# Kernel tuning notes

Measured on AMD Instinct MI355X. Metric: run time of the kernel, lower is better.

## Reference

```python
import jax, jax.numpy as jnp
import numpy as np

NUM_HEADS = 16


def setup_inputs() -> dict:
    key = jax.random.key(0)
    ks = jax.random.split(key, 9)
    B, S, C = 2, 2048, 1024
    s = 1.0 / np.sqrt(C)
    return {
        "hidden_states": jax.random.normal(ks[0], (B, S, C), jnp.float32),
        "Wq": jax.random.normal(ks[1], (C, C), jnp.float32) * s,
        "bq": jnp.zeros((C,), jnp.float32),
        "Wk": jax.random.normal(ks[2], (C, C), jnp.float32) * s,
        "bk": jnp.zeros((C,), jnp.float32),
        "Wv": jax.random.normal(ks[3], (C, C), jnp.float32) * s,
        "bv": jnp.zeros((C,), jnp.float32),
        "Wo": jax.random.normal(ks[4], (C, C), jnp.float32) * s,
        "bo": jnp.zeros((C,), jnp.float32),
    }


def reference(hidden_states, Wq, bq, Wk, bk, Wv, bv, Wo, bo):
    # Self-attention path of AttnProcessor (3D input, no mask, no norms,
    # residual_connection=True, rescale_output_factor=1.0).
    B, S, C = hidden_states.shape
    H = NUM_HEADS
    D = C // H
    residual = hidden_states

    q = hidden_states @ Wq + bq  # [B,S,C]
    k = hidden_states @ Wk + bk
    v = hidden_states @ Wv + bv

    # head_to_batch_dim: [B,S,C] -> [B,S,H,D]
    q = q.reshape(B, S, H, D)
    k = k.reshape(B, S, H, D)
    v = v.reshape(B, S, H, D)

    scale = 1.0 / np.sqrt(D).astype(np.float32)
    # get_attention_scores: baddbmm with scale, then softmax (full [B,H,S,S])
    scores = jnp.einsum("bqhd,bkhd->bhqk", q, k) * scale
    probs = jax.nn.softmax(scores, axis=-1)

    out = jnp.einsum("bhqk,bkhd->bqhd", probs, v)  # bmm(probs, value)
    out = out.reshape(B, S, C)  # batch_to_head_dim

    out = out @ Wo + bo  # to_out[0]; to_out[1] is dropout (identity in eval)
    out = out + residual  # residual_connection
    return out  # rescale_output_factor = 1.0
```

## Files before the change

### kernel.cpp

```cpp
#include <hip/hip_runtime.h>

#define BATCH 2
#define SEQ   2048
#define CH    1024
#define NHEAD 16
#define HDIM  64
#define MROWS (BATCH * SEQ)

typedef __attribute__((ext_vector_type(8))) short short8;
typedef __attribute__((ext_vector_type(4))) float floatx4;
typedef unsigned short ushort_t;

__device__ __forceinline__ float b2f(ushort_t u) {
    union { unsigned int i; float f; } x;
    x.i = ((unsigned int)u) << 16;
    return x.f;
}
__device__ __forceinline__ ushort_t f2b(float f) {
    union { float f; unsigned int i; } x;
    x.f = f;
    unsigned int lsb = (x.i >> 16) & 1u;
    x.i += 0x7fffu + lsb;
    return (ushort_t)(x.i >> 16);
}
__device__ __forceinline__ unsigned pack2(float a, float b) {
    return (unsigned)f2b(a) | ((unsigned)f2b(b) << 16);
}

__device__ __forceinline__ void gld16(const ushort_t* g, ushort_t* l) {
    __builtin_amdgcn_global_load_lds(
        (const __attribute__((address_space(1))) void*)g,
        (__attribute__((address_space(3))) void*)l, 16, 0, 0);
}

__global__ __launch_bounds__(256) void cvt_bf16_kernel(
    const float* __restrict__ in, ushort_t* __restrict__ out, int n4) {
    int i = blockIdx.x * blockDim.x + threadIdx.x;
    if (i < n4) {
        float4 v = ((const float4*)in)[i];
        ushort4 o = {f2b(v.x), f2b(v.y), f2b(v.z), f2b(v.w)};
        ((ushort4*)out)[i] = o;
    }
}

__global__ __launch_bounds__(256) void transpose_cvt_all(
    const float* __restrict__ W0, const float* __restrict__ W1,
    const float* __restrict__ W2, const float* __restrict__ W3,
    ushort_t* __restrict__ T0, ushort_t* __restrict__ T1,
    ushort_t* __restrict__ T2, ushort_t* __restrict__ T3) {
    __shared__ ushort_t T[64][68];
    const int z = blockIdx.z;
    const float* W = (z == 0) ? W0 : (z == 1) ? W1 : (z == 2) ? W2 : W3;
    ushort_t* Wt = (z == 0) ? T0 : (z == 1) ? T1 : (z == 2) ? T2 : T3;
    const int tid = threadIdx.x;
    const int n0 = blockIdx.x * 64, k0 = blockIdx.y * 64;
    const int r = tid >> 4, c4 = (tid & 15) * 4;
#pragma unroll
    for (int p = 0; p < 4; p++) {
        int k = p * 16 + r;
        float4 v = *(const float4*)&W[(size_t)(k0 + k) * CH + n0 + c4];
        T[c4 + 0][k] = f2b(v.x);
        T[c4 + 1][k] = f2b(v.y);
        T[c4 + 2][k] = f2b(v.z);
        T[c4 + 3][k] = f2b(v.w);
    }
    __syncthreads();
#pragma unroll
    for (int p = 0; p < 4; p++) {
        int n = p * 16 + r;
        ushort4 o = {T[n][c4 + 0], T[n][c4 + 1], T[n][c4 + 2], T[n][c4 + 3]};
        *(ushort4*)&Wt[(size_t)(n0 + n) * CH + k0 + c4] = o;
    }
}

__device__ __forceinline__ void gemm_core_db(
    const ushort_t* __restrict__ A, const ushort_t* __restrict__ Bt,
    int bm, int n0, int tid, floatx4 acc[4][4], ushort_t* lds) {
    const int wave = tid >> 6, lane = tid & 63;
    const int quad = lane >> 4, t16 = lane & 15;
    const int wm = wave >> 1, wn = wave & 1;
    const int arow = tid >> 2, ak = (tid & 3) * 8;

    const ushort_t* a0 = A + (size_t)(bm + arow) * CH + ak;
    const ushort_t* a1 = A + (size_t)(bm + 64 + arow) * CH + ak;
    const ushort_t* b0 = Bt + (size_t)(n0 + arow) * CH + ak;
    const ushort_t* b1 = Bt + (size_t)(n0 + 64 + arow) * CH + ak;

#pragma unroll
    for (int i = 0; i < 4; i++)
#pragma unroll
        for (int j = 0; j < 4; j++) acc[i][j] = (floatx4){0.f, 0.f, 0.f, 0.f};

    {
        ushort_t* As = lds;
        ushort_t* Bs = lds + 4096;
        gld16(a0, As + wave * 512);
        gld16(a1, As + 2048 + wave * 512);
        gld16(b0, Bs + wave * 512);
        gld16(b1, Bs + 2048 + wave * 512);
    }

    for (int it = 0; it < CH / 32; ++it) {
        __syncthreads();
        if (it + 1 < CH / 32) {
            ushort_t* nAs = lds + ((it + 1) & 1) * 8192;
            ushort_t* nBs = nAs + 4096;
            const int k = (it + 1) * 32;
            gld16(a0 + k, nAs + wave * 512);
            gld16(a1 + k, nAs + 2048 + wave * 512);
            gld16(b0 + k, nBs + wave * 512);
            gld16(b1 + k, nBs + 2048 + wave * 512);
        }
        const ushort_t* As = lds + (it & 1) * 8192;
        const ushort_t* Bs = As + 4096;
        short8 af[4], bf[4];
#pragma unroll
        for (int i = 0; i < 4; i++)
            af[i] = *(const short8*)&As[(wm * 64 + i * 16 + t16) * 32 + quad * 8];
#pragma unroll
        for (int j = 0; j < 4; j++)
            bf[j] = *(const short8*)&Bs[(wn * 64 + j * 16 + t16) * 32 + quad * 8];
#pragma unroll
        for (int i = 0; i < 4; i++)
#pragma unroll
            for (int j = 0; j < 4; j++)
                acc[i][j] = __builtin_amdgcn_mfma_f32_16x16x32_bf16(
                    af[i], bf[j], acc[i][j], 0, 0, 0);
    }
}

__global__ __launch_bounds__(256) void gemm_qkv(
    const ushort_t* __restrict__ X,
    const ushort_t* __restrict__ WqT, const ushort_t* __restrict__ WkT,
    const ushort_t* __restrict__ WvT,
    const float* __restrict__ bq, const float* __restrict__ bk,
    const float* __restrict__ bv,
    ushort_t* __restrict__ Qm, ushort_t* __restrict__ Km,
    ushort_t* __restrict__ Vtm) {
    __shared__ ushort_t lds[2 * 8192];
    const int tid = threadIdx.x;
    const int seg = blockIdx.x >> 3;
    const int n0 = (blockIdx.x & 7) * 128;
    const int bm = blockIdx.y * 128;
    const ushort_t* Bt = (seg == 0) ? WqT : (seg == 1) ? WkT : WvT;
    const float* bias = (seg == 0) ? bq : (seg == 1) ? bk : bv;

    floatx4 acc[4][4];
    gemm_core_db(X, Bt, bm, n0, tid, acc, lds);

    const int lane = tid & 63, wave = tid >> 6;
    const int quad = lane >> 4, t16 = lane & 15;
    const int wm = wave >> 1, wn = wave & 1;

    if (seg < 2) {
        ushort_t* outp = seg ? Km : Qm;
        const float sc = seg ? 1.0f : 0.125f;
#pragma unroll
        for (int i = 0; i < 4; i++)
#pragma unroll
            for (int j = 0; j < 4; j++) {
                const int col = n0 + wn * 64 + j * 16 + t16;
                const float bb = bias[col];
                const int row0 = bm + wm * 64 + i * 16 + quad * 4;
#pragma unroll
                for (int r = 0; r < 4; r++)
                    outp[(size_t)(row0 + r) * CH + col] =
                        f2b((acc[i][j][r] + bb) * sc);
            }
    } else {
        ushort_t* rep = lds;
        const int b = bm >> 11;
        const int s_base = bm & (SEQ - 1);
#pragma unroll
        for (int half = 0; half < 2; half++) {
            __syncthreads();
            if (wn == half) {
#pragma unroll
                for (int i = 0; i < 4; i++)
#pragma unroll
                    for (int j = 0; j < 4; j++) {
                        const int dl = j * 16 + t16;
                        const int sl = wm * 64 + i * 16 + quad * 4;
                        const float bb = bias[n0 + half * 64 + dl];
                        uint2 w = {pack2(acc[i][j][0] + bb, acc[i][j][1] + bb),
                                   pack2(acc[i][j][2] + bb, acc[i][j][3] + bb)};
                        *(uint2*)&rep[dl * 136 + sl] = w;
                    }
            }
            __syncthreads();
#pragma unroll
            for (int step = 0; step < 4; step++) {
                const int dl = step * 16 + (tid >> 4);
                const int sl = (tid & 15) * 8;
                short8 v = *(const short8*)&rep[dl * 136 + sl];
                const int col = n0 + half * 64 + dl;
                const int h = col >> 6, dd = col & 63;
                *(short8*)&Vtm[(((size_t)b * NHEAD + h) * HDIM + dd) * SEQ +
                               s_base + sl] = v;
            }
        }
    }
}

__global__ __launch_bounds__(256) void gemm_out(
    const ushort_t* __restrict__ Am, const ushort_t* __restrict__ WoT,
    const float* __restrict__ bo, const float* __restrict__ resid,
    float* __restrict__ out) {
    __shared__ ushort_t lds[2 * 6144];
    const int tid = threadIdx.x;
    const int n0 = blockIdx.x * 64;
    const int bm = blockIdx.y * 128;
    const int wave = tid >> 6, lane = tid & 63;
    const int quad = lane >> 4, t16 = lane & 15;
    const int arow = tid >> 2, ak = (tid & 3) * 8;

    const ushort_t* a0 = Am + (size_t)(bm + arow) * CH + ak;
    const ushort_t* a1 = Am + (size_t)(bm + 64 + arow) * CH + ak;
    const ushort_t* b0 = WoT + (size_t)(n0 + arow) * CH + ak;

    floatx4 acc[2][4];
#pragma unroll
    for (int i = 0; i < 2; i++)
#pragma unroll
        for (int j = 0; j < 4; j++) acc[i][j] = (floatx4){0.f, 0.f, 0.f, 0.f};

    {
        gld16(a0, lds + wave * 512);
        gld16(a1, lds + 2048 + wave * 512);
        gld16(b0, lds + 4096 + wave * 512);
    }

    for (int it = 0; it < CH / 32; ++it) {
        __syncthreads();
        if (it + 1 < CH / 32) {
            ushort_t* nAs = lds + ((it + 1) & 1) * 6144;
            const int k = (it + 1) * 32;
            gld16(a0 + k, nAs + wave * 512);
            gld16(a1 + k, nAs + 2048 + wave * 512);
            gld16(b0 + k, nAs + 4096 + wave * 512);
        }
        const ushort_t* As = lds + (it & 1) * 6144;
        const ushort_t* Bs = As + 4096;
        short8 af[2], bf[4];
#pragma unroll
        for (int i = 0; i < 2; i++)
            af[i] = *(const short8*)&As[(wave * 32 + i * 16 + t16) * 32 + quad * 8];
#pragma unroll
        for (int j = 0; j < 4; j++)
            bf[j] = *(const short8*)&Bs[(j * 16 + t16) * 32 + quad * 8];
#pragma unroll
        for (int i = 0; i < 2; i++)
#pragma unroll
            for (int j = 0; j < 4; j++)
                acc[i][j] = __builtin_amdgcn_mfma_f32_16x16x32_bf16(
                    af[i], bf[j], acc[i][j], 0, 0, 0);
    }

#pragma unroll
    for (int i = 0; i < 2; i++)
#pragma unroll
        for (int j = 0; j < 4; j++) {
            const int col = n0 + j * 16 + t16;
            const float bb = bo[col];
            const int row0 = bm + wave * 32 + i * 16 + quad * 4;
#pragma unroll
            for (int r = 0; r < 4; r++) {
                const size_t idx = (size_t)(row0 + r) * CH + col;
                out[idx] = acc[i][j][r] + bb + resid[idx];
            }
        }
}

__global__ __launch_bounds__(256, 4) void flash_attn_mfma(
    const ushort_t* __restrict__ Q, const ushort_t* __restrict__ K,
    const ushort_t* __restrict__ Vt, ushort_t* __restrict__ O) {
    __shared__ ushort_t Ks[64][72];
    __shared__ ushort_t Vs[64][72];
    __shared__ ushort_t Ps[4][32][72];

    const int tid = threadIdx.x;
    const int wave = tid >> 6, lane = tid & 63;
    const int quad = lane >> 4, t16 = lane & 15;
    const int bh = blockIdx.y, b = bh >> 4, h = bh & 15;
    const int q0 = blockIdx.x * 128;

    const size_t base_q = ((size_t)b * SEQ) * CH + (size_t)h * HDIM;
    const size_t base_vt = ((size_t)(b * NHEAD + h)) * HDIM * SEQ;

    short8 qf[2][2];
#pragma unroll
    for (int u = 0; u < 2; u++) {
        const ushort_t* qp =
            Q + base_q + (size_t)(q0 + wave * 32 + u * 16 + t16) * CH + quad * 8;
        qf[u][0] = *(const short8*)(qp);
        qf[u][1] = *(const short8*)(qp + 32);
    }

    const short8 ones = (short8)(short)0x3F80;

    floatx4 Oa[2][4];
    floatx4 Oe[2];
#pragma unroll
    for (int u = 0; u < 2; u++) {
        Oe[u] = (floatx4){0.f, 0.f, 0.f, 0.f};
#pragma unroll
        for (int d = 0; d < 4; d++) Oa[u][d] = (floatx4){0.f, 0.f, 0.f, 0.f};
    }

    const int r4 = tid >> 2;
    const int c16 = (tid & 3) * 16;

    for (int k0 = 0; k0 < SEQ; k0 += 64) {
        __syncthreads();
        {
            const ushort_t* kp = K + base_q + (size_t)(k0 + r4) * CH + c16;
            const ushort_t* vp = Vt + base_vt + (size_t)r4 * SEQ + k0 + c16;
            *(short8*)(&Ks[r4][c16]) = *(const short8*)(kp);
            *(short8*)(&Ks[r4][c16 + 8]) = *(const short8*)(kp + 8);
            *(short8*)(&Vs[r4][c16]) = *(const short8*)(vp);
            *(short8*)(&Vs[r4][c16 + 8]) = *(const short8*)(vp + 8);
        }
        __syncthreads();

#pragma unroll
        for (int j = 0; j < 4; j++) {
            short8 kf0 = *(const short8*)(&Ks[j * 16 + t16][quad * 8]);
            short8 kf1 = *(const short8*)(&Ks[j * 16 + t16][32 + quad * 8]);
#pragma unroll
            for (int u = 0; u < 2; u++) {
                floatx4 z = (floatx4){0.f, 0.f, 0.f, 0.f};
                z = __builtin_amdgcn_mfma_f32_16x16x32_bf16(qf[u][0], kf0, z, 0, 0, 0);
                z = __builtin_amdgcn_mfma_f32_16x16x32_bf16(qf[u][1], kf1, z, 0, 0, 0);
#pragma unroll
                for (int r = 0; r < 4; r++)
                    Ps[wave][u * 16 + quad * 4 + r][j * 16 + t16] =
                        f2b(__expf(z[r]));
            }
        }

        short8 pf[2][2];
#pragma unroll
        for (int u = 0; u < 2; u++) {
            pf[u][0] = *(const short8*)(&Ps[wave][u * 16 + t16][quad * 8]);
            pf[u][1] = *(const short8*)(&Ps[wave][u * 16 + t16][32 + quad * 8]);
        }
#pragma unroll
        for (int d = 0; d < 4; d++) {
            short8 vf0 = *(const short8*)(&Vs[d * 16 + t16][quad * 8]);
            short8 vf1 = *(const short8*)(&Vs[d * 16 + t16][32 + quad * 8]);
#pragma unroll
            for (int u = 0; u < 2; u++) {
                Oa[u][d] = __builtin_amdgcn_mfma_f32_16x16x32_bf16(
                    pf[u][0], vf0, Oa[u][d], 0, 0, 0);
                Oa[u][d] = __builtin_amdgcn_mfma_f32_16x16x32_bf16(
                    pf[u][1], vf1, Oa[u][d], 0, 0, 0);
            }
        }
#pragma unroll
        for (int u = 0; u < 2; u++) {
            Oe[u] = __builtin_amdgcn_mfma_f32_16x16x32_bf16(pf[u][0], ones, Oe[u], 0, 0, 0);
            Oe[u] = __builtin_amdgcn_mfma_f32_16x16x32_bf16(pf[u][1], ones, Oe[u], 0, 0, 0);
        }
    }

#pragma unroll
    for (int u = 0; u < 2; u++) {
        float inv[4];
#pragma unroll
        for (int r = 0; r < 4; r++) inv[r] = 1.f / Oe[u][r];
#pragma unroll
        for (int d = 0; d < 4; d++)
#pragma unroll
            for (int r = 0; r < 4; r++) {
                const int row = q0 + wave * 32 + u * 16 + quad * 4 + r;
                O[base_q + (size_t)row * CH + d * 16 + t16] =
                    f2b(Oa[u][d][r] * inv[r]);
            }
    }
}

extern "C" void kernel_launch(void* const* d_in, const int* in_sizes, int n_in,
                              void* d_out, int out_size, void* d_ws,
                              size_t ws_size, hipStream_t stream) {
    const float* X  = (const float*)d_in[0];
    const float* Wq = (const float*)d_in[1];
    const float* bq = (const float*)d_in[2];
    const float* Wk = (const float*)d_in[3];
    const float* bk = (const float*)d_in[4];
    const float* Wv = (const float*)d_in[5];
    const float* bv = (const float*)d_in[6];
    const float* Wo = (const float*)d_in[7];
    const float* bo = (const float*)d_in[8];
    float* out = (float*)d_out;

    const size_t MC = (size_t)MROWS * CH;
    const size_t WC = (size_t)CH * CH;
    ushort_t* ws  = (ushort_t*)d_ws;
    ushort_t* X16 = ws;
    ushort_t* Am  = ws;
    ushort_t* Qm  = ws + MC;
    ushort_t* Km  = ws + 2 * MC;
    ushort_t* Vtm = ws + 3 * MC;
    ushort_t* WqT = ws + 4 * MC;
    ushort_t* WkT = ws + 4 * MC + WC;
    ushort_t* WvT = ws + 4 * MC + 2 * WC;
    ushort_t* WoT = ws + 4 * MC + 3 * WC;

    dim3 blk(256);

    cvt_bf16_kernel<<<dim3((MC / 4 + 255) / 256), blk, 0, stream>>>(X, X16, (int)(MC / 4));
    transpose_cvt_all<<<dim3(16, 16, 4), blk, 0, stream>>>(
        Wq, Wk, Wv, Wo, WqT, WkT, WvT, WoT);

    gemm_qkv<<<dim3(24, 32), blk, 0, stream>>>(X16, WqT, WkT, WvT, bq, bk, bv,
                                               Qm, Km, Vtm);

    flash_attn_mfma<<<dim3(SEQ / 128, BATCH * NHEAD), blk, 0, stream>>>(Qm, Km, Vtm, Am);

    gemm_out<<<dim3(16, 32), blk, 0, stream>>>(Am, WoT, bo, X, out);
}
```

Baseline: 217.3 us.

## Restructure flash attention to 8 waves with register prefetch and transposed score MFMA

The attention kernel moves from 4 waves handling 32 query rows each to 8 waves handling 16 rows each, in 512-thread blocks. The next K/V tile is prefetched into registers while the current tile is computed, so global-load latency overlaps with math. Scores are computed as K·Q so each lane gets consecutive columns; these are packed with the hardware v_cvt_pk_bf16_f32 instruction and written to LDS as 8-byte stores instead of scalar 2-byte stores. s_setprio is raised around the PV MFMAs; the larger block with launch_bounds(512,4) may pressure registers and occupancy.

```diff
diff --git a/kernel.cpp b/kernel.cpp
--- a/kernel.cpp
+++ b/kernel.cpp
@@ -25,6 +25,11 @@
 }
 __device__ __forceinline__ unsigned pack2(float a, float b) {
     return (unsigned)f2b(a) | ((unsigned)f2b(b) << 16);
+}
+__device__ __forceinline__ unsigned cvt_pk_bf16(float a, float b) {
+    unsigned r;
+    asm("v_cvt_pk_bf16_f32 %0, %1, %2" : "=v"(r) : "v"(a), "v"(b));
+    return r;
 }
 
 __device__ __forceinline__ void gld16(const ushort_t* g, ushort_t* l) {
@@ -271,12 +276,12 @@
         }
 }
 
-__global__ __launch_bounds__(256, 4) void flash_attn_mfma(
+__global__ __launch_bounds__(512, 4) void flash_attn_mfma(
     const ushort_t* __restrict__ Q, const ushort_t* __restrict__ K,
     const ushort_t* __restrict__ Vt, ushort_t* __restrict__ O) {
     __shared__ ushort_t Ks[64][72];
     __shared__ ushort_t Vs[64][72];
-    __shared__ ushort_t Ps[4][32][72];
+    __shared__ ushort_t Ps[8][16][72];
 
     const int tid = threadIdx.x;
     const int wave = tid >> 6, lane = tid & 63;
@@ -287,96 +292,77 @@
     const size_t base_q = ((size_t)b * SEQ) * CH + (size_t)h * HDIM;
     const size_t base_vt = ((size_t)(b * NHEAD + h)) * HDIM * SEQ;
 
-    short8 qf[2][2];
-#pragma unroll
-    for (int u = 0; u < 2; u++) {
+    short8 qf[2];
+    {
         const ushort_t* qp =
-            Q + base_q + (size_t)(q0 + wave * 32 + u * 16 + t16) * CH + quad * 8;
-        qf[u][0] = *(const short8*)(qp);
-        qf[u][1] = *(const short8*)(qp + 32);
+            Q + base_q + (size_t)(q0 + wave * 16 + t16) * CH + quad * 8;
+        qf[0] = *(const short8*)(qp);
+        qf[1] = *(const short8*)(qp + 32);
     }
 
     const short8 ones = (short8)(short)0x3F80;
 
-    floatx4 Oa[2][4];
-    floatx4 Oe[2];
-#pragma unroll
-    for (int u = 0; u < 2; u++) {
-        Oe[u] = (floatx4){0.f, 0.f, 0.f, 0.f};
-#pragma unroll
-        for (int d = 0; d < 4; d++) Oa[u][d] = (floatx4){0.f, 0.f, 0.f, 0.f};
-    }
-
-    const int r4 = tid >> 2;
-    const int c16 = (tid & 3) * 16;
+    floatx4 Oa[4];
+    floatx4 Oe = (floatx4){0.f, 0.f, 0.f, 0.f};
+#pragma unroll
+    for (int d = 0; d < 4; d++) Oa[d] = (floatx4){0.f, 0.f, 0.f, 0.f};
+
+    const int r4 = tid >> 3;
+    const int c8 = (tid & 7) * 8;
+    const ushort_t* kp = K + base_q + (size_t)r4 * CH + c8;
+    const ushort_t* vp = Vt + base_vt + (size_t)r4 * SEQ + c8;
+
+    short8 kreg = *(const short8*)(kp);
+    short8 vreg = *(const short8*)(vp);
 
     for (int k0 = 0; k0 < SEQ; k0 += 64) {
         __syncthreads();
-        {
-            const ushort_t* kp = K + base_q + (size_t)(k0 + r4) * CH + c16;
-            const ushort_t* vp = Vt + base_vt + (size_t)r4 * SEQ + k0 + c16;
-            *(short8*)(&Ks[r4][c16]) = *(const short8*)(kp);
-            *(short8*)(&Ks[r4][c16 + 8]) = *(const short8*)(kp + 8);
-            *(short8*)(&Vs[r4][c16]) = *(const short8*)(vp);
-            *(short8*)(&Vs[r4][c16 + 8]) = *(const short8*)(vp + 8);
-        }
+        *(short8*)&Ks[r4][c8] = kreg;
+        *(short8*)&Vs[r4][c8] = vreg;
         __syncthreads();
+        if (k0 + 64 < SEQ) {
+            kreg = *(const short8*)(kp + (size_t)(k0 + 64) * CH);
+            vreg = *(const short8*)(vp + (k0 + 64));
+        }
 
 #pragma unroll
         for (int j = 0; j < 4; j++) {
             short8 kf0 = *(const short8*)(&Ks[j * 16 + t16][quad * 8]);
             short8 kf1 = *(const short8*)(&Ks[j * 16 + t16][32 + quad * 8]);
-#pragma unroll
-            for (int u = 0; u < 2; u++) {
-                floatx4 z = (floatx4){0.f, 0.f, 0.f, 0.f};
-                z = __builtin_amdgcn_mfma_f32_16x16x32_bf16(qf[u][0], kf0, z, 0, 0, 0);
-                z = __builtin_amdgcn_mfma_f32_16x16x32_bf16(qf[u][1], kf1, z, 0, 0, 0);
-#pragma unroll
-                for (int r = 0; r < 4; r++)
-                    Ps[wave][u * 16 + quad * 4 + r][j * 16 + t16] =
-                        f2b(__expf(z[r]));
-            }
-        }
-
-        short8 pf[2][2];
-#pragma unroll
-        for (int u = 0; u < 2; u++) {
-            pf[u][0] = *(const short8*)(&Ps[wave][u * 16 + t16][quad * 8]);
-            pf[u][1] = *(const short8*)(&Ps[wave][u * 16 + t16][32 + quad * 8]);
-        }
+            floatx4 z = (floatx4){0.f, 0.f, 0.f, 0.f};
+            z = __builtin_amdgcn_mfma_f32_16x16x32_bf16(kf0, qf[0], z, 0, 0, 0);
+            z = __builtin_amdgcn_mfma_f32_16x16x32_bf16(kf1, qf[1], z, 0, 0, 0);
+            uint2 w = {cvt_pk_bf16(__expf(z[0]), __expf(z[1])),
+                       cvt_pk_bf16(__expf(z[2]), __expf(z[3]))};
+            *(uint2*)&Ps[wave][t16][j * 16 + quad * 4] = w;
+        }
+
+        short8 pf0 = *(const short8*)(&Ps[wave][t16][quad * 8]);
+        short8 pf1 = *(const short8*)(&Ps[wave][t16][32 + quad * 8]);
+        __builtin_amdgcn_s_setprio(1);
 #pragma unroll
         for (int d = 0; d < 4; d++) {
             short8 vf0 = *(const short8*)(&Vs[d * 16 + t16][quad * 8]);
             short8 vf1 = *(const short8*)(&Vs[d * 16 + t16][32 + quad * 8]);
-#pragma unroll
-            for (int u = 0; u < 2; u++) {
-                Oa[u][d] = __builtin_amdgcn_mfma_f32_16x16x32_bf16(
-                    pf[u][0], vf0, Oa[u][d], 0, 0, 0);
-                Oa[u][d] = __builtin_amdgcn_mfma_f32_16x16x32_bf16(
-                    pf[u][1], vf1, Oa[u][d], 0, 0, 0);
-            }
-        }
-#pragma unroll
-        for (int u = 0; u < 2; u++) {
-            Oe[u] = __builtin_amdgcn_mfma_f32_16x16x32_bf16(pf[u][0], ones, Oe[u], 0, 0, 0);
-            Oe[u] = __builtin_amdgcn_mfma_f32_16x16x32_bf16(pf[u][1], ones, Oe[u], 0, 0, 0);
-        }
-    }
-
-#pragma unroll
-    for (int u = 0; u < 2; u++) {
-        float inv[4];
-#pragma unroll
-        for (int r = 0; r < 4; r++) inv[r] = 1.f / Oe[u][r];
-#pragma unroll
-        for (int d = 0; d < 4; d++)
-#pragma unroll
-            for (int r = 0; r < 4; r++) {
-                const int row = q0 + wave * 32 + u * 16 + quad * 4 + r;
-                O[base_q + (size_t)row * CH + d * 16 + t16] =
-                    f2b(Oa[u][d][r] * inv[r]);
-            }
-    }
+            Oa[d] = __builtin_amdgcn_mfma_f32_16x16x32_bf16(pf0, vf0, Oa[d], 0, 0, 0);
+            Oa[d] = __builtin_amdgcn_mfma_f32_16x16x32_bf16(pf1, vf1, Oa[d], 0, 0, 0);
+        }
+        Oe = __builtin_amdgcn_mfma_f32_16x16x32_bf16(pf0, ones, Oe, 0, 0, 0);
+        Oe = __builtin_amdgcn_mfma_f32_16x16x32_bf16(pf1, ones, Oe, 0, 0, 0);
+        __builtin_amdgcn_s_setprio(0);
+    }
+
+    float inv[4];
+#pragma unroll
+    for (int r = 0; r < 4; r++) inv[r] = 1.f / Oe[r];
+#pragma unroll
+    for (int d = 0; d < 4; d++)
+#pragma unroll
+        for (int r = 0; r < 4; r++) {
+            const int row = q0 + wave * 16 + quad * 4 + r;
+            O[base_q + (size_t)row * CH + d * 16 + t16] =
+                f2b(Oa[d][r] * inv[r]);
+        }
 }
 
 extern "C" void kernel_launch(void* const* d_in, const int* in_sizes, int n_in,
@@ -415,7 +401,8 @@
     gemm_qkv<<<dim3(24, 32), blk, 0, stream>>>(X16, WqT, WkT, WvT, bq, bk, bv,
                                                Qm, Km, Vtm);
 
-    flash_attn_mfma<<<dim3(SEQ / 128, BATCH * NHEAD), blk, 0, stream>>>(Qm, Km, Vtm, Am);
+    flash_attn_mfma<<<dim3(SEQ / 128, BATCH * NHEAD), dim3(512), 0, stream>>>(
+        Qm, Km, Vtm, Am);
 
     gemm_out<<<dim3(16, 32), blk, 0, stream>>>(Am, WoT, bo, X, out);
 }
```

After: 209.2 us. 3.7% less time.

## Keep attention probabilities in registers and prefetch next K/V tile

Applied to the files above, without the earlier changes.

The attention kernel swaps the MFMA operand order so each lane's score outputs line up with the register layout needed for the P·V MFMA. The probabilities are packed with v_cvt_pk_bf16_f32 and fed directly, which removes the per-wave P shared-memory round trip. To match that layout, V columns are written into LDS in a permuted order. The next K/V tile is loaded into registers while the current one is computed, and the MFMA section runs at raised wave priority. This adds register pressure and depends on the permutation being exactly right for correctness.

```diff
diff --git a/kernel.cpp b/kernel.cpp
--- a/kernel.cpp
+++ b/kernel.cpp
@@ -25,6 +25,11 @@
 }
 __device__ __forceinline__ unsigned pack2(float a, float b) {
     return (unsigned)f2b(a) | ((unsigned)f2b(b) << 16);
+}
+__device__ __forceinline__ unsigned cvt_pk_bf16(float a, float b) {
+    unsigned r;
+    asm("v_cvt_pk_bf16_f32 %0, %1, %2" : "=v"(r) : "v"(a), "v"(b));
+    return r;
 }
 
 __device__ __forceinline__ void gld16(const ushort_t* g, ushort_t* l) {
@@ -276,7 +281,6 @@
     const ushort_t* __restrict__ Vt, ushort_t* __restrict__ O) {
     __shared__ ushort_t Ks[64][72];
     __shared__ ushort_t Vs[64][72];
-    __shared__ ushort_t Ps[4][32][72];
 
     const int tid = threadIdx.x;
     const int wave = tid >> 6, lane = tid & 63;
@@ -308,20 +312,43 @@
     }
 
     const int r4 = tid >> 2;
-    const int c16 = (tid & 3) * 16;
+    const int t4 = tid & 3;
+    const ushort_t* kp = K + base_q + (size_t)r4 * CH + t4 * 8;
+    const ushort_t* vp = Vt + base_vt + (size_t)r4 * SEQ + t4 * 8;
+
+    const int c0 = t4, c1 = t4 + 4;
+    const int v00 = ((c0 & 4) << 3) + (((2 * c0) & 3) << 3) + (((c0 >> 1) & 1) << 2);
+    const int v01 = ((c0 & 4) << 3) + (((2 * c0 + 1) & 3) << 3) + (((c0 >> 1) & 1) << 2);
+    const int v10 = ((c1 & 4) << 3) + (((2 * c1) & 3) << 3) + (((c1 >> 1) & 1) << 2);
+    const int v11 = ((c1 & 4) << 3) + (((2 * c1 + 1) & 3) << 3) + (((c1 >> 1) & 1) << 2);
+
+    short8 kr0 = *(const short8*)(kp);
+    short8 kr1 = *(const short8*)(kp + 32);
+    short8 vr0 = *(const short8*)(vp);
+    short8 vr1 = *(const short8*)(vp + 32);
 
     for (int k0 = 0; k0 < SEQ; k0 += 64) {
         __syncthreads();
+        *(short8*)&Ks[r4][t4 * 8] = kr0;
+        *(short8*)&Ks[r4][t4 * 8 + 32] = kr1;
         {
-            const ushort_t* kp = K + base_q + (size_t)(k0 + r4) * CH + c16;
-            const ushort_t* vp = Vt + base_vt + (size_t)r4 * SEQ + k0 + c16;
-            *(short8*)(&Ks[r4][c16]) = *(const short8*)(kp);
-            *(short8*)(&Ks[r4][c16 + 8]) = *(const short8*)(kp + 8);
-            *(short8*)(&Vs[r4][c16]) = *(const short8*)(vp);
-            *(short8*)(&Vs[r4][c16 + 8]) = *(const short8*)(vp + 8);
+            union { short8 s; uint4 u; } va, vb;
+            va.s = vr0; vb.s = vr1;
+            *(uint2*)&Vs[r4][v00] = (uint2){va.u.x, va.u.y};
+            *(uint2*)&Vs[r4][v01] = (uint2){va.u.z, va.u.w};
+            *(uint2*)&Vs[r4][v10] = (uint2){vb.u.x, vb.u.y};
+            *(uint2*)&Vs[r4][v11] = (uint2){vb.u.z, vb.u.w};
         }
         __syncthreads();
-
+        if (k0 + 64 < SEQ) {
+            const ushort_t* nkp = kp + (size_t)(k0 + 64) * CH;
+            kr0 = *(const short8*)(nkp);
+            kr1 = *(const short8*)(nkp + 32);
+            vr0 = *(const short8*)(vp + (k0 + 64));
+            vr1 = *(const short8*)(vp + (k0 + 64) + 32);
+        }
+
+        unsigned pk[2][8];
 #pragma unroll
         for (int j = 0; j < 4; j++) {
             short8 kf0 = *(const short8*)(&Ks[j * 16 + t16][quad * 8]);
@@ -329,31 +356,31 @@
 #pragma unroll
             for (int u = 0; u < 2; u++) {
                 floatx4 z = (floatx4){0.f, 0.f, 0.f, 0.f};
-                z = __builtin_amdgcn_mfma_f32_16x16x32_bf16(qf[u][0], kf0, z, 0, 0, 0);
-                z = __builtin_amdgcn_mfma_f32_16x16x32_bf16(qf[u][1], kf1, z, 0, 0, 0);
-#pragma unroll
-                for (int r = 0; r < 4; r++)
-                    Ps[wave][u * 16 + quad * 4 + r][j * 16 + t16] =
-                        f2b(__expf(z[r]));
-            }
-        }
-
+                z = __builtin_amdgcn_mfma_f32_16x16x32_bf16(kf0, qf[u][0], z, 0, 0, 0);
+                z = __builtin_amdgcn_mfma_f32_16x16x32_bf16(kf1, qf[u][1], z, 0, 0, 0);
+                pk[u][j * 2] = cvt_pk_bf16(__expf(z[0]), __expf(z[1]));
+                pk[u][j * 2 + 1] = cvt_pk_bf16(__expf(z[2]), __expf(z[3]));
+            }
+        }
         short8 pf[2][2];
 #pragma unroll
         for (int u = 0; u < 2; u++) {
-            pf[u][0] = *(const short8*)(&Ps[wave][u * 16 + t16][quad * 8]);
-            pf[u][1] = *(const short8*)(&Ps[wave][u * 16 + t16][32 + quad * 8]);
-        }
+            union { uint4 q; short8 s; } cc;
+            cc.q = (uint4){pk[u][0], pk[u][1], pk[u][2], pk[u][3]};
+            pf[u][0] = cc.s;
+            cc.q = (uint4){pk[u][4], pk[u][5], pk[u][6], pk[u][7]};
+            pf[u][1] = cc.s;
+        }
+
+        __builtin_amdgcn_s_setprio(1);
 #pragma unroll
         for (int d = 0; d < 4; d++) {
             short8 vf0 = *(const short8*)(&Vs[d * 16 + t16][quad * 8]);
             short8 vf1 = *(const short8*)(&Vs[d * 16 + t16][32 + quad * 8]);
 #pragma unroll
             for (int u = 0; u < 2; u++) {
-                Oa[u][d] = __builtin_amdgcn_mfma_f32_16x16x32_bf16(
-                    pf[u][0], vf0, Oa[u][d], 0, 0, 0);
-                Oa[u][d] = __builtin_amdgcn_mfma_f32_16x16x32_bf16(
-                    pf[u][1], vf1, Oa[u][d], 0, 0, 0);
+                Oa[u][d] = __builtin_amdgcn_mfma_f32_16x16x32_bf16(pf[u][0], vf0, Oa[u][d], 0, 0, 0);
+                Oa[u][d] = __builtin_amdgcn_mfma_f32_16x16x32_bf16(pf[u][1], vf1, Oa[u][d], 0, 0, 0);
             }
         }
 #pragma unroll
@@ -361,6 +388,7 @@
             Oe[u] = __builtin_amdgcn_mfma_f32_16x16x32_bf16(pf[u][0], ones, Oe[u], 0, 0, 0);
             Oe[u] = __builtin_amdgcn_mfma_f32_16x16x32_bf16(pf[u][1], ones, Oe[u], 0, 0, 0);
         }
+        __builtin_amdgcn_s_setprio(0);
     }
 
 #pragma unroll
@@ -415,7 +443,8 @@
     gemm_qkv<<<dim3(24, 32), blk, 0, stream>>>(X16, WqT, WkT, WvT, bq, bk, bv,
                                                Qm, Km, Vtm);
 
-    flash_attn_mfma<<<dim3(SEQ / 128, BATCH * NHEAD), blk, 0, stream>>>(Qm, Km, Vtm, Am);
+    flash_attn_mfma<<<dim3(SEQ / 128, BATCH * NHEAD), blk, 0, stream>>>(
+        Qm, Km, Vtm, Am);
 
     gemm_out<<<dim3(16, 32), blk, 0, stream>>>(Am, WoT, bo, X, out);
 }
```

Result: faster. 198.2 us (-8.8%).
